# Kernel tuning notes

Hardware: AMD Instinct MI355X
Metric: run time of the kernel (lower is better)

Reference implementation:

```python
import jax, jax.numpy as jnp
import numpy as np

K = 512
N = 65536
BN_EPS = 1e-5


def setup_inputs() -> dict:
    key = jax.random.key(0)
    kx, = jax.random.split(key, 1)
    X = jax.random.normal(kx, (N, K), dtype=jnp.float32)
    C1 = jnp.eye(K, dtype=jnp.float32)
    C2 = jnp.ones((K,), dtype=jnp.float32)
    C3 = jnp.zeros((1,), dtype=jnp.float32)
    return {"X": X, "C1": C1, "C2": C2, "C3": C3}


def reference(X, C1, C2, C3):
    # diag(X @ C1 @ X.T) == sum((X @ C1) * X, axis=-1)  (row-wise quadratic form)
    quad = jnp.einsum("nk,kj,nj->n", X, C1, X)  # [N]
    y = quad[:, None] + C2 * X + C3              # [N, K]
    # BatchNorm1d (training mode, affine=False): biased batch stats per feature
    mean = jnp.mean(y, axis=0)
    var = jnp.mean((y - mean) ** 2, axis=0)
    return (y - mean) / jnp.sqrt(var + BN_EPS)
```

## Files before the change

### kernel.cpp

```cpp
#include <hip/hip_runtime.h>
#include <hip/hip_bf16.h>

#define NROWS 65536
#define KDIM  512
constexpr float BN_EPS = 1e-5f;

using short8 = __attribute__((ext_vector_type(8))) short;
using f32x4  = __attribute__((ext_vector_type(4))) float;

#define BM 128

__device__ __forceinline__ void gload_lds16(const void* g, void* l) {
  __builtin_amdgcn_global_load_lds(
      (const __attribute__((address_space(1))) void*)g,
      (__attribute__((address_space(3))) void*)l, 16, 0, 0);
}

__device__ __forceinline__ short bf16bits(float x) {
  __hip_bfloat16 h = __float2bfloat16(x);
  return *reinterpret_cast<short*>(&h);
}
__device__ __forceinline__ short8 cvt8(const float4& a, const float4& b) {
  short8 h;
  h[0] = bf16bits(a.x); h[1] = bf16bits(a.y); h[2] = bf16bits(a.z); h[3] = bf16bits(a.w);
  h[4] = bf16bits(b.x); h[5] = bf16bits(b.y); h[6] = bf16bits(b.z); h[7] = bf16bits(b.w);
  return h;
}

__global__ __launch_bounds__(256)
void prep_c1(const float* __restrict__ C1, short8* __restrict__ c1tH) {
  const int e   = blockIdx.x * 256 + threadIdx.x;
  const int col = e & 511;
  const int kg  = e >> 9;
  short8 hi;
  #pragma unroll
  for (int i = 0; i < 8; ++i)
    hi[i] = bf16bits(C1[(size_t)(kg * 8 + i) * KDIM + col]);
  c1tH[e] = hi;
}

__global__ __launch_bounds__(512, 2)
void quad_kernel(const float* __restrict__ X, const short8* __restrict__ c1tH,
                 float* __restrict__ quad,
                 float* __restrict__ colS1, float* __restrict__ colS2,
                 float* __restrict__ colS3, double* __restrict__ qsumsA) {
  __shared__ short8 Bs[3][2048];
  __shared__ float  As[3][4096];
  __shared__ float qPart[4][BM];
  __shared__ float qLds[BM];

  const int tid  = threadIdx.x;
  const int lane = tid & 63;
  const int w    = tid >> 6;
  const int wr   = w >> 2;
  const int wc   = w & 3;
  const int g    = lane >> 4;
  const int lr   = lane & 15;
  const int bid  = blockIdx.x;
  const int r0   = bid * BM;

  const int arow = tid >> 3;
  const int ac   = tid & 7;
  const float* asrc0 = X + (size_t)(r0 + arow) * KDIM + ((ac ^ (arow & 7)) * 4);
  const float* asrc1 = asrc0 + (size_t)64 * KDIM;

#define STAGE(bufi, kt)                                                    \
  {                                                                        \
    gload_lds16(c1tH + (kt) * 2048 + tid,        &Bs[bufi][tid]);          \
    gload_lds16(c1tH + (kt) * 2048 + 512 + tid,  &Bs[bufi][512 + tid]);    \
    gload_lds16(c1tH + (kt) * 2048 + 1024 + tid, &Bs[bufi][1024 + tid]);   \
    gload_lds16(c1tH + (kt) * 2048 + 1536 + tid, &Bs[bufi][1536 + tid]);   \
    gload_lds16(asrc0 + (kt) * 32, &As[bufi][tid * 4]);                    \
    gload_lds16(asrc1 + (kt) * 32, &As[bufi][(512 + tid) * 4]);            \
  }

  f32x4 acc[4][8];
  #pragma unroll
  for (int rf = 0; rf < 4; ++rf)
    #pragma unroll
    for (int cf = 0; cf < 8; ++cf)
      acc[rf][cf] = (f32x4){0.f, 0.f, 0.f, 0.f};

  STAGE(0, 0);
  STAGE(1, 1);
  asm volatile("s_waitcnt vmcnt(6)" ::: "memory");
  __builtin_amdgcn_s_barrier();
  __builtin_amdgcn_sched_barrier(0);

  #pragma unroll
  for (int kt = 0; kt < 16; ++kt) {
    const int buf = kt % 3;
    if (kt < 14) STAGE((kt + 2) % 3, kt + 2);
    short8 Af[4];
    #pragma unroll
    for (int rf = 0; rf < 4; ++rf) {
      const int row = wr * 64 + rf * 16 + lr;
      const float4 x0 = *(const float4*)&As[buf][row * 32 + (((2 * g) ^ (row & 7)) * 4)];
      const float4 x1 = *(const float4*)&As[buf][row * 32 + (((2 * g + 1) ^ (row & 7)) * 4)];
      Af[rf] = cvt8(x0, x1);
    }
    const int fb = g * 512 + wc * 128 + lr;
    {
      const short8 b0 = Bs[buf][fb];
      const short8 b1 = Bs[buf][fb + 16];
      const short8 b2 = Bs[buf][fb + 32];
      const short8 b3 = Bs[buf][fb + 48];
      #pragma unroll
      for (int rf = 0; rf < 4; ++rf) {
        acc[rf][0] = __builtin_amdgcn_mfma_f32_16x16x32_bf16(Af[rf], b0, acc[rf][0], 0, 0, 0);
        acc[rf][1] = __builtin_amdgcn_mfma_f32_16x16x32_bf16(Af[rf], b1, acc[rf][1], 0, 0, 0);
        acc[rf][2] = __builtin_amdgcn_mfma_f32_16x16x32_bf16(Af[rf], b2, acc[rf][2], 0, 0, 0);
        acc[rf][3] = __builtin_amdgcn_mfma_f32_16x16x32_bf16(Af[rf], b3, acc[rf][3], 0, 0, 0);
      }
    }
    {
      const short8 b4 = Bs[buf][fb + 64];
      const short8 b5 = Bs[buf][fb + 80];
      const short8 b6 = Bs[buf][fb + 96];
      const short8 b7 = Bs[buf][fb + 112];
      #pragma unroll
      for (int rf = 0; rf < 4; ++rf) {
        acc[rf][4] = __builtin_amdgcn_mfma_f32_16x16x32_bf16(Af[rf], b4, acc[rf][4], 0, 0, 0);
        acc[rf][5] = __builtin_amdgcn_mfma_f32_16x16x32_bf16(Af[rf], b5, acc[rf][5], 0, 0, 0);
        acc[rf][6] = __builtin_amdgcn_mfma_f32_16x16x32_bf16(Af[rf], b6, acc[rf][6], 0, 0, 0);
        acc[rf][7] = __builtin_amdgcn_mfma_f32_16x16x32_bf16(Af[rf], b7, acc[rf][7], 0, 0, 0);
      }
    }
    if (kt < 14) {
      asm volatile("s_waitcnt vmcnt(6)" ::: "memory");
    } else if (kt == 14) {
      asm volatile("s_waitcnt vmcnt(0)" ::: "memory");
    }
    if (kt < 15) {
      __builtin_amdgcn_s_barrier();
      __builtin_amdgcn_sched_barrier(0);
    }
  }
#undef STAGE

  #pragma unroll
  for (int rf = 0; rf < 4; ++rf)
    #pragma unroll
    for (int p = 0; p < 4; ++p) {
      const int row = wr * 64 + rf * 16 + g * 4 + p;
      const float* xr = X + (size_t)(r0 + row) * KDIM + wc * 128;
      float s = 0.f;
      #pragma unroll
      for (int cf = 0; cf < 8; ++cf)
        s += acc[rf][cf][p] * xr[cf * 16 + lr];
      s += __shfl_xor(s, 1, 64);
      s += __shfl_xor(s, 2, 64);
      s += __shfl_xor(s, 4, 64);
      s += __shfl_xor(s, 8, 64);
      if (lr == 0) qPart[wc][row] = s;
    }
  __syncthreads();
  if (tid < BM) {
    const float q = qPart[0][tid] + qPart[1][tid] + qPart[2][tid] + qPart[3][tid];
    quad[r0 + tid] = q;
    qLds[tid] = q;
  }
  __syncthreads();
  {
    const int cb = (bid & 3) * 512;
    float s1 = 0.f, s2 = 0.f, s3 = 0.f;
    for (int r = 0; r < BM; ++r) {
      const float q = qLds[r];
      const float x = X[(size_t)(r0 + r) * KDIM + tid];
      s1 += x; s2 += x * x; s3 += q * x;
    }
    atomicAdd(&colS1[cb + tid], s1);
    atomicAdd(&colS2[cb + tid], s2);
    atomicAdd(&colS3[cb + tid], s3);
  }
  if (tid < BM) {
    double q = (double)qLds[tid];
    double q2 = q * q;
    #pragma unroll
    for (int m = 1; m < 64; m <<= 1) {
      q  += __shfl_xor(q,  m, 64);
      q2 += __shfl_xor(q2, m, 64);
    }
    if ((tid & 63) == 0) {
      atomicAdd(&qsumsA[(bid & 31) * 2],     q);
      atomicAdd(&qsumsA[(bid & 31) * 2 + 1], q2);
    }
  }
}

__global__ void finalize_kernel(const float* __restrict__ colS1, const float* __restrict__ colS2,
                                const float* __restrict__ colS3, const double* __restrict__ qsumsA,
                                const float* __restrict__ C2, const float* __restrict__ C3,
                                float* __restrict__ mean, float* __restrict__ inv_std) {
  __shared__ double sQ[2];
  if (threadIdx.x == 0) {
    double a = 0.0, b = 0.0;
    for (int i = 0; i < 32; ++i) { a += qsumsA[2 * i]; b += qsumsA[2 * i + 1]; }
    sQ[0] = a; sQ[1] = b;
  }
  __syncthreads();
  const int k = blockIdx.x * blockDim.x + threadIdx.x;
  if (k >= KDIM) return;
  const double invN = 1.0 / (double)NROWS;
  const double meanQ = sQ[0] * invN;
  const double varQ  = sQ[1] * invN - meanQ * meanQ;
  const float meanX = (colS1[k] + colS1[k + 512] + colS1[k + 1024] + colS1[k + 1536]) * (float)invN;
  const float s2    = (colS2[k] + colS2[k + 512] + colS2[k + 1024] + colS2[k + 1536]) * (float)invN;
  const float s3    = (colS3[k] + colS3[k + 512] + colS3[k + 1024] + colS3[k + 1536]) * (float)invN;
  const float varX  = s2 - meanX * meanX;
  const float covQX = s3 - (float)meanQ * meanX;
  const float c2 = C2[k];
  const float c3 = C3[0];
  const float m = (float)meanQ + c2 * meanX + c3;
  const float v = (float)varQ + c2 * c2 * varX + 2.0f * c2 * covQX;
  mean[k] = m;
  inv_std[k] = 1.0f / sqrtf(v + BN_EPS);
}

__global__ __launch_bounds__(256)
void normalize_kernel(const float* __restrict__ X, const float* __restrict__ quad,
                      const float* __restrict__ C2, const float* __restrict__ C3,
                      const float* __restrict__ mean, const float* __restrict__ inv_std,
                      float* __restrict__ out) {
  const int idx = blockIdx.x * blockDim.x + threadIdx.x;
  const int n = idx >> 7;
  const int j4 = idx & 127;
  const float q = quad[n];
  const float c3 = C3[0];
  const float4 x  = *(const float4*)&X[(size_t)idx * 4];
  const float4 c2 = *(const float4*)&C2[j4 * 4];
  const float4 m  = *(const float4*)&mean[j4 * 4];
  const float4 iv = *(const float4*)&inv_std[j4 * 4];
  float4 o;
  o.x = (q + c2.x * x.x + c3 - m.x) * iv.x;
  o.y = (q + c2.y * x.y + c3 - m.y) * iv.y;
  o.z = (q + c2.z * x.z + c3 - m.z) * iv.z;
  o.w = (q + c2.w * x.w + c3 - m.w) * iv.w;
  *(float4*)&out[(size_t)idx * 4] = o;
}

extern "C" void kernel_launch(void* const* d_in, const int* in_sizes, int n_in,
                              void* d_out, int out_size, void* d_ws, size_t ws_size,
                              hipStream_t stream) {
  const float* X  = (const float*)d_in[0];
  const float* C1 = (const float*)d_in[1];
  const float* C2 = (const float*)d_in[2];
  const float* C3 = (const float*)d_in[3];
  float* out = (float*)d_out;

  char* ws = (char*)d_ws;
  float*  quad    = (float*)ws;
  float*  colS1   = (float*)(ws + 262144);
  float*  colS2   = (float*)(ws + 262144 + 8192);
  float*  colS3   = (float*)(ws + 262144 + 16384);
  double* qsumsA  = (double*)(ws + 262144 + 24576);
  float*  mean    = (float*)(ws + 262144 + 25088);
  float*  inv_std = (float*)(ws + 262144 + 27136);
  short8* c1tH    = (short8*)(ws + 294912);

  hipMemsetAsync(colS1, 0, 24576 + 512, stream);

  prep_c1<<<128, 256, 0, stream>>>(C1, c1tH);
  quad_kernel<<<NROWS / BM, 512, 0, stream>>>(X, c1tH, quad,
                                              colS1, colS2, colS3, qsumsA);
  finalize_kernel<<<2, 256, 0, stream>>>(colS1, colS2, colS3, qsumsA, C2, C3, mean, inv_std);
  normalize_kernel<<<(NROWS * (KDIM / 4)) / 256, 256, 0, stream>>>(
      X, quad, C2, C3, mean, inv_std, out);
}
```

Baseline: 120.7 us.

## Split quad GEMM across two column halves per row block with bf16 A staging

```diff
diff --git a/kernel.cpp b/kernel.cpp
--- a/kernel.cpp
+++ b/kernel.cpp
@@ -29,23 +29,26 @@
 
 __global__ __launch_bounds__(256)
 void prep_c1(const float* __restrict__ C1, short8* __restrict__ c1tH) {
-  const int e   = blockIdx.x * 256 + threadIdx.x;
-  const int col = e & 511;
-  const int kg  = e >> 9;
+  const int e  = blockIdx.x * 256 + threadIdx.x;
+  const int kt = e >> 11;
+  const int jh = (e >> 10) & 1;
+  const int g  = (e >> 8) & 3;
+  const int c  = e & 255;
+  const int col = jh * 256 + c;
   short8 hi;
   #pragma unroll
   for (int i = 0; i < 8; ++i)
-    hi[i] = bf16bits(C1[(size_t)(kg * 8 + i) * KDIM + col]);
+    hi[i] = bf16bits(C1[(size_t)((kt * 4 + g) * 8 + i) * KDIM + col]);
   c1tH[e] = hi;
 }
 
-__global__ __launch_bounds__(512, 2)
+__global__ __launch_bounds__(512, 4)
 void quad_kernel(const float* __restrict__ X, const short8* __restrict__ c1tH,
                  float* __restrict__ quad,
                  float* __restrict__ colS1, float* __restrict__ colS2,
-                 float* __restrict__ colS3, double* __restrict__ qsumsA) {
-  __shared__ short8 Bs[3][2048];
-  __shared__ float  As[3][4096];
+                 float* __restrict__ colS3) {
+  __shared__ short8 Bs[3][1024];
+  __shared__ short8 Asb[2][512];
   __shared__ float qPart[4][BM];
   __shared__ float qLds[BM];
 
@@ -57,97 +60,91 @@
   const int g    = lane >> 4;
   const int lr   = lane & 15;
   const int bid  = blockIdx.x;
-  const int r0   = bid * BM;
-
-  const int arow = tid >> 3;
-  const int ac   = tid & 7;
-  const float* asrc0 = X + (size_t)(r0 + arow) * KDIM + ((ac ^ (arow & 7)) * 4);
-  const float* asrc1 = asrc0 + (size_t)64 * KDIM;
-
-#define STAGE(bufi, kt)                                                    \
+  const int p    = bid >> 1;
+  const int jh   = bid & 1;
+  const int r0   = p * BM;
+
+  const short8* bsrc = c1tH + jh * 1024;
+  const int arow = tid >> 2;
+  const int ac   = tid & 3;
+  const float* asrc = X + (size_t)(r0 + arow) * KDIM + ac * 8;
+  const int adst = ac * 128 + arow;
+
+#define STAGE_B(kt)                                                        \
   {                                                                        \
-    gload_lds16(c1tH + (kt) * 2048 + tid,        &Bs[bufi][tid]);          \
-    gload_lds16(c1tH + (kt) * 2048 + 512 + tid,  &Bs[bufi][512 + tid]);    \
-    gload_lds16(c1tH + (kt) * 2048 + 1024 + tid, &Bs[bufi][1024 + tid]);   \
-    gload_lds16(c1tH + (kt) * 2048 + 1536 + tid, &Bs[bufi][1536 + tid]);   \
-    gload_lds16(asrc0 + (kt) * 32, &As[bufi][tid * 4]);                    \
-    gload_lds16(asrc1 + (kt) * 32, &As[bufi][(512 + tid) * 4]);            \
-  }
-
-  f32x4 acc[4][8];
+    gload_lds16(bsrc + (kt) * 2048 + tid,       &Bs[(kt) % 3][tid]);       \
+    gload_lds16(bsrc + (kt) * 2048 + 512 + tid, &Bs[(kt) % 3][512 + tid]); \
+  }
+
+  f32x4 acc[4][4];
   #pragma unroll
   for (int rf = 0; rf < 4; ++rf)
     #pragma unroll
-    for (int cf = 0; cf < 8; ++cf)
+    for (int cf = 0; cf < 4; ++cf)
       acc[rf][cf] = (f32x4){0.f, 0.f, 0.f, 0.f};
 
-  STAGE(0, 0);
-  STAGE(1, 1);
-  asm volatile("s_waitcnt vmcnt(6)" ::: "memory");
-  __builtin_amdgcn_s_barrier();
-  __builtin_amdgcn_sched_barrier(0);
+  {
+    float4 a0 = *(const float4*)(asrc);
+    float4 a1 = *(const float4*)(asrc + 4);
+    STAGE_B(0);
+    STAGE_B(1);
+    asm volatile("s_waitcnt vmcnt(2)" ::: "memory");
+    Asb[0][adst] = cvt8(a0, a1);
+    asm volatile("s_waitcnt lgkmcnt(0)" ::: "memory");
+    __builtin_amdgcn_s_barrier();
+    __builtin_amdgcn_sched_barrier(0);
+  }
 
   #pragma unroll
   for (int kt = 0; kt < 16; ++kt) {
     const int buf = kt % 3;
-    if (kt < 14) STAGE((kt + 2) % 3, kt + 2);
+    float4 nr0, nr1;
+    if (kt < 15) {
+      nr0 = *(const float4*)(asrc + (kt + 1) * 32);
+      nr1 = *(const float4*)(asrc + (kt + 1) * 32 + 4);
+    }
+    if (kt < 14) STAGE_B(kt + 2);
+
     short8 Af[4];
     #pragma unroll
+    for (int rf = 0; rf < 4; ++rf)
+      Af[rf] = Asb[kt & 1][g * 128 + wr * 64 + rf * 16 + lr];
+    const int fb = g * 256 + wc * 64 + lr;
+    const short8 b0 = Bs[buf][fb];
+    const short8 b1 = Bs[buf][fb + 16];
+    const short8 b2 = Bs[buf][fb + 32];
+    const short8 b3 = Bs[buf][fb + 48];
+    #pragma unroll
     for (int rf = 0; rf < 4; ++rf) {
-      const int row = wr * 64 + rf * 16 + lr;
-      const float4 x0 = *(const float4*)&As[buf][row * 32 + (((2 * g) ^ (row & 7)) * 4)];
-      const float4 x1 = *(const float4*)&As[buf][row * 32 + (((2 * g + 1) ^ (row & 7)) * 4)];
-      Af[rf] = cvt8(x0, x1);
-    }
-    const int fb = g * 512 + wc * 128 + lr;
-    {
-      const short8 b0 = Bs[buf][fb];
-      const short8 b1 = Bs[buf][fb + 16];
-      const short8 b2 = Bs[buf][fb + 32];
-      const short8 b3 = Bs[buf][fb + 48];
-      #pragma unroll
-      for (int rf = 0; rf < 4; ++rf) {
-        acc[rf][0] = __builtin_amdgcn_mfma_f32_16x16x32_bf16(Af[rf], b0, acc[rf][0], 0, 0, 0);
-        acc[rf][1] = __builtin_amdgcn_mfma_f32_16x16x32_bf16(Af[rf], b1, acc[rf][1], 0, 0, 0);
-        acc[rf][2] = __builtin_amdgcn_mfma_f32_16x16x32_bf16(Af[rf], b2, acc[rf][2], 0, 0, 0);
-        acc[rf][3] = __builtin_amdgcn_mfma_f32_16x16x32_bf16(Af[rf], b3, acc[rf][3], 0, 0, 0);
+      acc[rf][0] = __builtin_amdgcn_mfma_f32_16x16x32_bf16(Af[rf], b0, acc[rf][0], 0, 0, 0);
+      acc[rf][1] = __builtin_amdgcn_mfma_f32_16x16x32_bf16(Af[rf], b1, acc[rf][1], 0, 0, 0);
+      acc[rf][2] = __builtin_amdgcn_mfma_f32_16x16x32_bf16(Af[rf], b2, acc[rf][2], 0, 0, 0);
+      acc[rf][3] = __builtin_amdgcn_mfma_f32_16x16x32_bf16(Af[rf], b3, acc[rf][3], 0, 0, 0);
+    }
+    if (kt < 15) {
+      if (kt < 14) {
+        asm volatile("s_waitcnt vmcnt(2)" ::: "memory");
+      } else {
+        asm volatile("s_waitcnt vmcnt(0)" ::: "memory");
       }
-    }
-    {
-      const short8 b4 = Bs[buf][fb + 64];
-      const short8 b5 = Bs[buf][fb + 80];
-      const short8 b6 = Bs[buf][fb + 96];
-      const short8 b7 = Bs[buf][fb + 112];
-      #pragma unroll
-      for (int rf = 0; rf < 4; ++rf) {
-        acc[rf][4] = __builtin_amdgcn_mfma_f32_16x16x32_bf16(Af[rf], b4, acc[rf][4], 0, 0, 0);
-        acc[rf][5] = __builtin_amdgcn_mfma_f32_16x16x32_bf16(Af[rf], b5, acc[rf][5], 0, 0, 0);
-        acc[rf][6] = __builtin_amdgcn_mfma_f32_16x16x32_bf16(Af[rf], b6, acc[rf][6], 0, 0, 0);
-        acc[rf][7] = __builtin_amdgcn_mfma_f32_16x16x32_bf16(Af[rf], b7, acc[rf][7], 0, 0, 0);
-      }
-    }
-    if (kt < 14) {
-      asm volatile("s_waitcnt vmcnt(6)" ::: "memory");
-    } else if (kt == 14) {
-      asm volatile("s_waitcnt vmcnt(0)" ::: "memory");
-    }
-    if (kt < 15) {
+      Asb[(kt + 1) & 1][adst] = cvt8(nr0, nr1);
+      asm volatile("s_waitcnt lgkmcnt(0)" ::: "memory");
       __builtin_amdgcn_s_barrier();
       __builtin_amdgcn_sched_barrier(0);
     }
   }
-#undef STAGE
+#undef STAGE_B
 
   #pragma unroll
   for (int rf = 0; rf < 4; ++rf)
     #pragma unroll
-    for (int p = 0; p < 4; ++p) {
-      const int row = wr * 64 + rf * 16 + g * 4 + p;
-      const float* xr = X + (size_t)(r0 + row) * KDIM + wc * 128;
+    for (int pp = 0; pp < 4; ++pp) {
+      const int row = wr * 64 + rf * 16 + g * 4 + pp;
+      const float* xr = X + (size_t)(r0 + row) * KDIM + jh * 256 + wc * 64;
       float s = 0.f;
       #pragma unroll
-      for (int cf = 0; cf < 8; ++cf)
-        s += acc[rf][cf][p] * xr[cf * 16 + lr];
+      for (int cf = 0; cf < 4; ++cf)
+        s += acc[rf][cf][pp] * xr[cf * 16 + lr];
       s += __shfl_xor(s, 1, 64);
       s += __shfl_xor(s, 2, 64);
       s += __shfl_xor(s, 4, 64);
@@ -157,7 +154,7 @@
   __syncthreads();
   if (tid < BM) {
     const float q = qPart[0][tid] + qPart[1][tid] + qPart[2][tid] + qPart[3][tid];
-    quad[r0 + tid] = q;
+    atomicAdd(&quad[r0 + tid], q);
     qLds[tid] = q;
   }
   __syncthreads();
@@ -169,22 +166,29 @@
       const float x = X[(size_t)(r0 + r) * KDIM + tid];
       s1 += x; s2 += x * x; s3 += q * x;
     }
-    atomicAdd(&colS1[cb + tid], s1);
-    atomicAdd(&colS2[cb + tid], s2);
     atomicAdd(&colS3[cb + tid], s3);
-  }
-  if (tid < BM) {
-    double q = (double)qLds[tid];
-    double q2 = q * q;
-    #pragma unroll
-    for (int m = 1; m < 64; m <<= 1) {
-      q  += __shfl_xor(q,  m, 64);
-      q2 += __shfl_xor(q2, m, 64);
-    }
-    if ((tid & 63) == 0) {
-      atomicAdd(&qsumsA[(bid & 31) * 2],     q);
-      atomicAdd(&qsumsA[(bid & 31) * 2 + 1], q2);
-    }
+    if (jh == 0) {
+      atomicAdd(&colS1[cb + tid], s1);
+      atomicAdd(&colS2[cb + tid], s2);
+    }
+  }
+}
+
+__global__ __launch_bounds__(256)
+void qreduce_kernel(const float* __restrict__ quad, double* __restrict__ qsumsA) {
+  const int idx = blockIdx.x * 256 + threadIdx.x;
+  const float4 q4 = *(const float4*)&quad[idx * 4];
+  double s  = (double)q4.x + (double)q4.y + (double)q4.z + (double)q4.w;
+  double s2 = (double)q4.x * q4.x + (double)q4.y * q4.y +
+              (double)q4.z * q4.z + (double)q4.w * q4.w;
+  #pragma unroll
+  for (int m = 1; m < 64; m <<= 1) {
+    s  += __shfl_xor(s,  m, 64);
+    s2 += __shfl_xor(s2, m, 64);
+  }
+  if ((threadIdx.x & 63) == 0) {
+    atomicAdd(&qsumsA[0], s);
+    atomicAdd(&qsumsA[1], s2);
   }
 }
 
@@ -192,18 +196,11 @@
                                 const float* __restrict__ colS3, const double* __restrict__ qsumsA,
                                 const float* __restrict__ C2, const float* __restrict__ C3,
                                 float* __restrict__ mean, float* __restrict__ inv_std) {
-  __shared__ double sQ[2];
-  if (threadIdx.x == 0) {
-    double a = 0.0, b = 0.0;
-    for (int i = 0; i < 32; ++i) { a += qsumsA[2 * i]; b += qsumsA[2 * i + 1]; }
-    sQ[0] = a; sQ[1] = b;
-  }
-  __syncthreads();
   const int k = blockIdx.x * blockDim.x + threadIdx.x;
   if (k >= KDIM) return;
   const double invN = 1.0 / (double)NROWS;
-  const double meanQ = sQ[0] * invN;
-  const double varQ  = sQ[1] * invN - meanQ * meanQ;
+  const double meanQ = qsumsA[0] * invN;
+  const double varQ  = qsumsA[1] * invN - meanQ * meanQ;
   const float meanX = (colS1[k] + colS1[k + 512] + colS1[k + 1024] + colS1[k + 1536]) * (float)invN;
   const float s2    = (colS2[k] + colS2[k + 512] + colS2[k + 1024] + colS2[k + 1536]) * (float)invN;
   const float s3    = (colS3[k] + colS3[k + 512] + colS3[k + 1024] + colS3[k + 1536]) * (float)invN;
@@ -258,11 +255,12 @@
   float*  inv_std = (float*)(ws + 262144 + 27136);
   short8* c1tH    = (short8*)(ws + 294912);
 
-  hipMemsetAsync(colS1, 0, 24576 + 512, stream);
+  hipMemsetAsync(ws, 0, 262144 + 24576 + 512, stream);
 
   prep_c1<<<128, 256, 0, stream>>>(C1, c1tH);
-  quad_kernel<<<NROWS / BM, 512, 0, stream>>>(X, c1tH, quad,
-                                              colS1, colS2, colS3, qsumsA);
+  quad_kernel<<<(NROWS / BM) * 2, 512, 0, stream>>>(X, c1tH, quad,
+                                                    colS1, colS2, colS3);
+  qreduce_kernel<<<64, 256, 0, stream>>>(quad, qsumsA);
   finalize_kernel<<<2, 256, 0, stream>>>(colS1, colS2, colS3, qsumsA, C2, C3, mean, inv_std);
   normalize_kernel<<<(NROWS * (KDIM / 4)) / 256, 256, 0, stream>>>(
       X, quad, C2, C3, mean, inv_std, out);
```

Result: slower. 152.0 us (+26.0%).

## Use 1024-thread blocks with register-loaded A fragments and double-buffered B

Applied to the files above, without the earlier changes.

```diff
diff --git a/kernel.cpp b/kernel.cpp
--- a/kernel.cpp
+++ b/kernel.cpp
@@ -39,111 +39,112 @@
   c1tH[e] = hi;
 }
 
-__global__ __launch_bounds__(512, 2)
+__global__ __launch_bounds__(1024)
 void quad_kernel(const float* __restrict__ X, const short8* __restrict__ c1tH,
                  float* __restrict__ quad,
                  float* __restrict__ colS1, float* __restrict__ colS2,
                  float* __restrict__ colS3, double* __restrict__ qsumsA) {
-  __shared__ short8 Bs[3][2048];
-  __shared__ float  As[3][4096];
-  __shared__ float qPart[4][BM];
+  __shared__ short8 Bs[2][2048];
+  __shared__ float qPart[8][BM];
   __shared__ float qLds[BM];
 
   const int tid  = threadIdx.x;
   const int lane = tid & 63;
   const int w    = tid >> 6;
-  const int wr   = w >> 2;
-  const int wc   = w & 3;
+  const int wr   = w >> 3;
+  const int wc   = w & 7;
   const int g    = lane >> 4;
   const int lr   = lane & 15;
   const int bid  = blockIdx.x;
   const int r0   = bid * BM;
 
-  const int arow = tid >> 3;
-  const int ac   = tid & 7;
-  const float* asrc0 = X + (size_t)(r0 + arow) * KDIM + ((ac ^ (arow & 7)) * 4);
-  const float* asrc1 = asrc0 + (size_t)64 * KDIM;
-
-#define STAGE(bufi, kt)                                                    \
+  const int wrr = w >> 2;
+  const int wcc = w & 3;
+  const float* asrc0 = X + (size_t)(r0 + wrr * 32 + lr) * KDIM + g * 8;
+  const float* asrc1 = asrc0 + 16 * KDIM;
+
+#define LOADA(kt, dst)                                  \
+  {                                                     \
+    dst[0] = *(const float4*)(asrc0 + (kt) * 32);       \
+    dst[1] = *(const float4*)(asrc0 + (kt) * 32 + 4);   \
+    dst[2] = *(const float4*)(asrc1 + (kt) * 32);       \
+    dst[3] = *(const float4*)(asrc1 + (kt) * 32 + 4);   \
+  }
+#define STAGE_B(bufi, kt)                                                  \
   {                                                                        \
     gload_lds16(c1tH + (kt) * 2048 + tid,        &Bs[bufi][tid]);          \
-    gload_lds16(c1tH + (kt) * 2048 + 512 + tid,  &Bs[bufi][512 + tid]);    \
     gload_lds16(c1tH + (kt) * 2048 + 1024 + tid, &Bs[bufi][1024 + tid]);   \
-    gload_lds16(c1tH + (kt) * 2048 + 1536 + tid, &Bs[bufi][1536 + tid]);   \
-    gload_lds16(asrc0 + (kt) * 32, &As[bufi][tid * 4]);                    \
-    gload_lds16(asrc1 + (kt) * 32, &As[bufi][(512 + tid) * 4]);            \
-  }
-
-  f32x4 acc[4][8];
-  #pragma unroll
-  for (int rf = 0; rf < 4; ++rf)
+  }
+
+  f32x4 acc[2][8];
+  #pragma unroll
+  for (int rf = 0; rf < 2; ++rf)
     #pragma unroll
     for (int cf = 0; cf < 8; ++cf)
       acc[rf][cf] = (f32x4){0.f, 0.f, 0.f, 0.f};
 
-  STAGE(0, 0);
-  STAGE(1, 1);
-  asm volatile("s_waitcnt vmcnt(6)" ::: "memory");
+  float4 ae[4], ao[4];
+
+  LOADA(0, ae);
+  STAGE_B(0, 0);
+  asm volatile("s_waitcnt vmcnt(0)" ::: "memory");
   __builtin_amdgcn_s_barrier();
   __builtin_amdgcn_sched_barrier(0);
 
   #pragma unroll
   for (int kt = 0; kt < 16; ++kt) {
-    const int buf = kt % 3;
-    if (kt < 14) STAGE((kt + 2) % 3, kt + 2);
-    short8 Af[4];
-    #pragma unroll
-    for (int rf = 0; rf < 4; ++rf) {
-      const int row = wr * 64 + rf * 16 + lr;
-      const float4 x0 = *(const float4*)&As[buf][row * 32 + (((2 * g) ^ (row & 7)) * 4)];
-      const float4 x1 = *(const float4*)&As[buf][row * 32 + (((2 * g + 1) ^ (row & 7)) * 4)];
-      Af[rf] = cvt8(x0, x1);
-    }
-    const int fb = g * 512 + wc * 128 + lr;
+    const int buf = kt & 1;
+    if (kt < 15) {
+      if (kt & 1) { LOADA(kt + 1, ae); } else { LOADA(kt + 1, ao); }
+      STAGE_B(buf ^ 1, kt + 1);
+    }
+    short8 A0, A1;
+    if (kt & 1) { A0 = cvt8(ao[0], ao[1]); A1 = cvt8(ao[2], ao[3]); }
+    else        { A0 = cvt8(ae[0], ae[1]); A1 = cvt8(ae[2], ae[3]); }
+    const int fb = g * 512 + wcc * 128 + lr;
     {
       const short8 b0 = Bs[buf][fb];
       const short8 b1 = Bs[buf][fb + 16];
       const short8 b2 = Bs[buf][fb + 32];
       const short8 b3 = Bs[buf][fb + 48];
-      #pragma unroll
-      for (int rf = 0; rf < 4; ++rf) {
-        acc[rf][0] = __builtin_amdgcn_mfma_f32_16x16x32_bf16(Af[rf], b0, acc[rf][0], 0, 0, 0);
-        acc[rf][1] = __builtin_amdgcn_mfma_f32_16x16x32_bf16(Af[rf], b1, acc[rf][1], 0, 0, 0);
-        acc[rf][2] = __builtin_amdgcn_mfma_f32_16x16x32_bf16(Af[rf], b2, acc[rf][2], 0, 0, 0);
-        acc[rf][3] = __builtin_amdgcn_mfma_f32_16x16x32_bf16(Af[rf], b3, acc[rf][3], 0, 0, 0);
-      }
+      acc[0][0] = __builtin_amdgcn_mfma_f32_16x16x32_bf16(A0, b0, acc[0][0], 0, 0, 0);
+      acc[1][0] = __builtin_amdgcn_mfma_f32_16x16x32_bf16(A1, b0, acc[1][0], 0, 0, 0);
+      acc[0][1] = __builtin_amdgcn_mfma_f32_16x16x32_bf16(A0, b1, acc[0][1], 0, 0, 0);
+      acc[1][1] = __builtin_amdgcn_mfma_f32_16x16x32_bf16(A1, b1, acc[1][1], 0, 0, 0);
+      acc[0][2] = __builtin_amdgcn_mfma_f32_16x16x32_bf16(A0, b2, acc[0][2], 0, 0, 0);
+      acc[1][2] = __builtin_amdgcn_mfma_f32_16x16x32_bf16(A1, b2, acc[1][2], 0, 0, 0);
+      acc[0][3] = __builtin_amdgcn_mfma_f32_16x16x32_bf16(A0, b3, acc[0][3], 0, 0, 0);
+      acc[1][3] = __builtin_amdgcn_mfma_f32_16x16x32_bf16(A1, b3, acc[1][3], 0, 0, 0);
     }
     {
       const short8 b4 = Bs[buf][fb + 64];
       const short8 b5 = Bs[buf][fb + 80];
       const short8 b6 = Bs[buf][fb + 96];
       const short8 b7 = Bs[buf][fb + 112];
-      #pragma unroll
-      for (int rf = 0; rf < 4; ++rf) {
-        acc[rf][4] = __builtin_amdgcn_mfma_f32_16x16x32_bf16(Af[rf], b4, acc[rf][4], 0, 0, 0);
-        acc[rf][5] = __builtin_amdgcn_mfma_f32_16x16x32_bf16(Af[rf], b5, acc[rf][5], 0, 0, 0);
-        acc[rf][6] = __builtin_amdgcn_mfma_f32_16x16x32_bf16(Af[rf], b6, acc[rf][6], 0, 0, 0);
-        acc[rf][7] = __builtin_amdgcn_mfma_f32_16x16x32_bf16(Af[rf], b7, acc[rf][7], 0, 0, 0);
-      }
-    }
-    if (kt < 14) {
-      asm volatile("s_waitcnt vmcnt(6)" ::: "memory");
-    } else if (kt == 14) {
+      acc[0][4] = __builtin_amdgcn_mfma_f32_16x16x32_bf16(A0, b4, acc[0][4], 0, 0, 0);
+      acc[1][4] = __builtin_amdgcn_mfma_f32_16x16x32_bf16(A1, b4, acc[1][4], 0, 0, 0);
+      acc[0][5] = __builtin_amdgcn_mfma_f32_16x16x32_bf16(A0, b5, acc[0][5], 0, 0, 0);
+      acc[1][5] = __builtin_amdgcn_mfma_f32_16x16x32_bf16(A1, b5, acc[1][5], 0, 0, 0);
+      acc[0][6] = __builtin_amdgcn_mfma_f32_16x16x32_bf16(A0, b6, acc[0][6], 0, 0, 0);
+      acc[1][6] = __builtin_amdgcn_mfma_f32_16x16x32_bf16(A1, b6, acc[1][6], 0, 0, 0);
+      acc[0][7] = __builtin_amdgcn_mfma_f32_16x16x32_bf16(A0, b7, acc[0][7], 0, 0, 0);
+      acc[1][7] = __builtin_amdgcn_mfma_f32_16x16x32_bf16(A1, b7, acc[1][7], 0, 0, 0);
+    }
+    if (kt < 15) {
       asm volatile("s_waitcnt vmcnt(0)" ::: "memory");
-    }
-    if (kt < 15) {
       __builtin_amdgcn_s_barrier();
       __builtin_amdgcn_sched_barrier(0);
     }
   }
-#undef STAGE
-
-  #pragma unroll
-  for (int rf = 0; rf < 4; ++rf)
+#undef LOADA
+#undef STAGE_B
+
+  #pragma unroll
+  for (int rf = 0; rf < 2; ++rf)
     #pragma unroll
     for (int p = 0; p < 4; ++p) {
-      const int row = wr * 64 + rf * 16 + g * 4 + p;
-      const float* xr = X + (size_t)(r0 + row) * KDIM + wc * 128;
+      const int row = wrr * 32 + rf * 16 + g * 4 + p;
+      const float* xr = X + (size_t)(r0 + row) * KDIM + wcc * 128;
       float s = 0.f;
       #pragma unroll
       for (int cf = 0; cf < 8; ++cf)
@@ -152,7 +153,9 @@
       s += __shfl_xor(s, 2, 64);
       s += __shfl_xor(s, 4, 64);
       s += __shfl_xor(s, 8, 64);
-      if (lr == 0) qPart[wc][row] = s;
+      if (lr == 0) {
+        qPart[wcc][row] = s;
+      }
     }
   __syncthreads();
   if (tid < BM) {
@@ -162,16 +165,18 @@
   }
   __syncthreads();
   {
-    const int cb = (bid & 3) * 512;
+    const int col   = tid & 511;
+    const int rbase = (tid >> 9) * 64;
+    const int cb    = (bid & 3) * 512;
     float s1 = 0.f, s2 = 0.f, s3 = 0.f;
-    for (int r = 0; r < BM; ++r) {
+    for (int r = rbase; r < rbase + 64; ++r) {
       const float q = qLds[r];
-      const float x = X[(size_t)(r0 + r) * KDIM + tid];
+      const float x = X[(size_t)(r0 + r) * KDIM + col];
       s1 += x; s2 += x * x; s3 += q * x;
     }
-    atomicAdd(&colS1[cb + tid], s1);
-    atomicAdd(&colS2[cb + tid], s2);
-    atomicAdd(&colS3[cb + tid], s3);
+    atomicAdd(&colS1[cb + col], s1);
+    atomicAdd(&colS2[cb + col], s2);
+    atomicAdd(&colS3[cb + col], s3);
   }
   if (tid < BM) {
     double q = (double)qLds[tid];
@@ -261,8 +266,8 @@
   hipMemsetAsync(colS1, 0, 24576 + 512, stream);
 
   prep_c1<<<128, 256, 0, stream>>>(C1, c1tH);
-  quad_kernel<<<NROWS / BM, 512, 0, stream>>>(X, c1tH, quad,
-                                              colS1, colS2, colS3, qsumsA);
+  quad_kernel<<<NROWS / BM, 1024, 0, stream>>>(X, c1tH, quad,
+                                               colS1, colS2, colS3, qsumsA);
   finalize_kernel<<<2, 256, 0, stream>>>(colS1, colS2, colS3, qsumsA, C2, C3, mean, inv_std);
   normalize_kernel<<<(NROWS * (KDIM / 4)) / 256, 256, 0, stream>>>(
       X, quad, C2, C3, mean, inv_std, out);
```

After: 170.2 us. 41.1% more time.

## Load X directly into registers and double-buffer B with larger K steps

Applied to the files above, without the earlier changes.

```diff
diff --git a/kernel.cpp b/kernel.cpp
--- a/kernel.cpp
+++ b/kernel.cpp
@@ -44,8 +44,7 @@
                  float* __restrict__ quad,
                  float* __restrict__ colS1, float* __restrict__ colS2,
                  float* __restrict__ colS3, double* __restrict__ qsumsA) {
-  __shared__ short8 Bs[3][2048];
-  __shared__ float  As[3][4096];
+  __shared__ short8 Bs[2][4096];
   __shared__ float qPart[4][BM];
   __shared__ float qLds[BM];
 
@@ -59,19 +58,33 @@
   const int bid  = blockIdx.x;
   const int r0   = bid * BM;
 
-  const int arow = tid >> 3;
-  const int ac   = tid & 7;
-  const float* asrc0 = X + (size_t)(r0 + arow) * KDIM + ((ac ^ (arow & 7)) * 4);
-  const float* asrc1 = asrc0 + (size_t)64 * KDIM;
-
-#define STAGE(bufi, kt)                                                    \
+  const float* abase = X + (size_t)(r0 + wr * 64 + lr) * KDIM + g * 8;
+
+#define LOADA(k)                                                           \
   {                                                                        \
-    gload_lds16(c1tH + (kt) * 2048 + tid,        &Bs[bufi][tid]);          \
-    gload_lds16(c1tH + (kt) * 2048 + 512 + tid,  &Bs[bufi][512 + tid]);    \
-    gload_lds16(c1tH + (kt) * 2048 + 1024 + tid, &Bs[bufi][1024 + tid]);   \
-    gload_lds16(c1tH + (kt) * 2048 + 1536 + tid, &Bs[bufi][1536 + tid]);   \
-    gload_lds16(asrc0 + (kt) * 32, &As[bufi][tid * 4]);                    \
-    gload_lds16(asrc1 + (kt) * 32, &As[bufi][(512 + tid) * 4]);            \
+    _Pragma("unroll")                                                      \
+    for (int rf = 0; rf < 4; ++rf) {                                       \
+      const float* ap = abase + rf * (16 * KDIM) + (k) * 64;               \
+      raw[rf][0][0] = *(const float4*)(ap);                                \
+      raw[rf][0][1] = *(const float4*)(ap + 4);                            \
+      raw[rf][1][0] = *(const float4*)(ap + 32);                           \
+      raw[rf][1][1] = *(const float4*)(ap + 36);                           \
+    }                                                                      \
+  }
+#define STAGE_B(bufi, k)                                                   \
+  {                                                                        \
+    _Pragma("unroll")                                                      \
+    for (int s = 0; s < 8; ++s)                                            \
+      gload_lds16(c1tH + (k) * 4096 + s * 512 + tid,                       \
+                  &Bs[bufi][s * 512 + tid]);                               \
+  }
+#define CVTA()                                                             \
+  {                                                                        \
+    _Pragma("unroll")                                                      \
+    for (int rf = 0; rf < 4; ++rf) {                                       \
+      Af[rf][0] = cvt8(raw[rf][0][0], raw[rf][0][1]);                      \
+      Af[rf][1] = cvt8(raw[rf][1][0], raw[rf][1][1]);                      \
+    }                                                                      \
   }
 
   f32x4 acc[4][8];
@@ -81,62 +94,58 @@
     for (int cf = 0; cf < 8; ++cf)
       acc[rf][cf] = (f32x4){0.f, 0.f, 0.f, 0.f};
 
-  STAGE(0, 0);
-  STAGE(1, 1);
-  asm volatile("s_waitcnt vmcnt(6)" ::: "memory");
+  float4 raw[4][2][2];
+  short8 Af[4][2];
+
+  LOADA(0);
+  STAGE_B(0, 0);
+  asm volatile("s_waitcnt vmcnt(8)" ::: "memory");
+  CVTA();
+  asm volatile("s_waitcnt vmcnt(0)" ::: "memory");
   __builtin_amdgcn_s_barrier();
   __builtin_amdgcn_sched_barrier(0);
 
   #pragma unroll
-  for (int kt = 0; kt < 16; ++kt) {
-    const int buf = kt % 3;
-    if (kt < 14) STAGE((kt + 2) % 3, kt + 2);
-    short8 Af[4];
-    #pragma unroll
-    for (int rf = 0; rf < 4; ++rf) {
-      const int row = wr * 64 + rf * 16 + lr;
-      const float4 x0 = *(const float4*)&As[buf][row * 32 + (((2 * g) ^ (row & 7)) * 4)];
-      const float4 x1 = *(const float4*)&As[buf][row * 32 + (((2 * g + 1) ^ (row & 7)) * 4)];
-      Af[rf] = cvt8(x0, x1);
-    }
-    const int fb = g * 512 + wc * 128 + lr;
-    {
+  for (int k = 0; k < 8; ++k) {
+    const int buf = k & 1;
+    if (k < 7) {
+      LOADA(k + 1);
+      STAGE_B(buf ^ 1, k + 1);
+    }
+    #pragma unroll
+    for (int sub = 0; sub < 2; ++sub) {
+      const int fb = sub * 2048 + g * 512 + wc * 128 + lr;
       const short8 b0 = Bs[buf][fb];
       const short8 b1 = Bs[buf][fb + 16];
       const short8 b2 = Bs[buf][fb + 32];
       const short8 b3 = Bs[buf][fb + 48];
-      #pragma unroll
-      for (int rf = 0; rf < 4; ++rf) {
-        acc[rf][0] = __builtin_amdgcn_mfma_f32_16x16x32_bf16(Af[rf], b0, acc[rf][0], 0, 0, 0);
-        acc[rf][1] = __builtin_amdgcn_mfma_f32_16x16x32_bf16(Af[rf], b1, acc[rf][1], 0, 0, 0);
-        acc[rf][2] = __builtin_amdgcn_mfma_f32_16x16x32_bf16(Af[rf], b2, acc[rf][2], 0, 0, 0);
-        acc[rf][3] = __builtin_amdgcn_mfma_f32_16x16x32_bf16(Af[rf], b3, acc[rf][3], 0, 0, 0);
-      }
-    }
-    {
       const short8 b4 = Bs[buf][fb + 64];
       const short8 b5 = Bs[buf][fb + 80];
       const short8 b6 = Bs[buf][fb + 96];
       const short8 b7 = Bs[buf][fb + 112];
       #pragma unroll
       for (int rf = 0; rf < 4; ++rf) {
-        acc[rf][4] = __builtin_amdgcn_mfma_f32_16x16x32_bf16(Af[rf], b4, acc[rf][4], 0, 0, 0);
-        acc[rf][5] = __builtin_amdgcn_mfma_f32_16x16x32_bf16(Af[rf], b5, acc[rf][5], 0, 0, 0);
-        acc[rf][6] = __builtin_amdgcn_mfma_f32_16x16x32_bf16(Af[rf], b6, acc[rf][6], 0, 0, 0);
-        acc[rf][7] = __builtin_amdgcn_mfma_f32_16x16x32_bf16(Af[rf], b7, acc[rf][7], 0, 0, 0);
+        acc[rf][0] = __builtin_amdgcn_mfma_f32_16x16x32_bf16(Af[rf][sub], b0, acc[rf][0], 0, 0, 0);
+        acc[rf][1] = __builtin_amdgcn_mfma_f32_16x16x32_bf16(Af[rf][sub], b1, acc[rf][1], 0, 0, 0);
+        acc[rf][2] = __builtin_amdgcn_mfma_f32_16x16x32_bf16(Af[rf][sub], b2, acc[rf][2], 0, 0, 0);
+        acc[rf][3] = __builtin_amdgcn_mfma_f32_16x16x32_bf16(Af[rf][sub], b3, acc[rf][3], 0, 0, 0);
+        acc[rf][4] = __builtin_amdgcn_mfma_f32_16x16x32_bf16(Af[rf][sub], b4, acc[rf][4], 0, 0, 0);
+        acc[rf][5] = __builtin_amdgcn_mfma_f32_16x16x32_bf16(Af[rf][sub], b5, acc[rf][5], 0, 0, 0);
+        acc[rf][6] = __builtin_amdgcn_mfma_f32_16x16x32_bf16(Af[rf][sub], b6, acc[rf][6], 0, 0, 0);
+        acc[rf][7] = __builtin_amdgcn_mfma_f32_16x16x32_bf16(Af[rf][sub], b7, acc[rf][7], 0, 0, 0);
       }
     }
-    if (kt < 14) {
-      asm volatile("s_waitcnt vmcnt(6)" ::: "memory");
-    } else if (kt == 14) {
+    if (k < 7) {
+      asm volatile("s_waitcnt vmcnt(8)" ::: "memory");
+      CVTA();
       asm volatile("s_waitcnt vmcnt(0)" ::: "memory");
-    }
-    if (kt < 15) {
       __builtin_amdgcn_s_barrier();
       __builtin_amdgcn_sched_barrier(0);
     }
   }
-#undef STAGE
+#undef LOADA
+#undef STAGE_B
+#undef CVTA
 
   #pragma unroll
   for (int rf = 0; rf < 4; ++rf)
```

Result: slower. 184.6 us (+53.0%).
